# Kernel optimization log

Hardware: AMD Instinct MI355X
Metric: run time of the kernel (lower is better)

Reference implementation:

```python
import jax, jax.numpy as jnp
import numpy as np

B, C, H, W = 64, 32, 112, 112
RANK = 3


def setup_inputs() -> dict:
    key = jax.random.key(0)
    k1, k2, k3, k4, k5 = jax.random.split(key, 5)
    N = H * W  # 12544
    return {
        "x": jax.random.uniform(k1, (B, C, H, W), dtype=jnp.float32),
        "p_buffer": jax.random.normal(k2, (B, N, RANK), dtype=jnp.float32),
        "q_buffer": jax.random.normal(k3, (B, C, RANK), dtype=jnp.float32),
        "grad_p_buffer": jax.random.normal(k4, (B, N, RANK), dtype=jnp.float32),
        "grad_q_buffer": jax.random.normal(k5, (B, C, RANK), dtype=jnp.float32),
        "n_iter": 2,
    }


def _power_svd(X, P, Q, n_iter):
    # X: [b, c, n]; P: [b, n, r]; Q: [b, c, r]
    for i in range(n_iter):
        if i == n_iter - 1:
            P = jnp.linalg.qr(P)[0]  # batched reduced QR, tall-skinny (n x r)
        Q = jnp.einsum('bcn,bnr->bcr', X, P)
        if i == n_iter - 1:
            Q = jnp.linalg.qr(Q)[0]  # batched reduced QR (c x r)
        P = jnp.einsum('bcn,bcr->bnr', X, Q)  # X^T @ Q
    return P, Q


def reference(x, p_buffer, q_buffer, grad_p_buffer, grad_q_buffer, n_iter):
    shape = x.shape
    X = x.reshape(shape[0], shape[1], -1)  # [B, C, H*W]
    P, Q = _power_svd(X, p_buffer, q_buffer, n_iter)
    # low-rank reconstruction Q @ P^T, back to original shape
    return jnp.einsum('bcr,bnr->bcn', Q, P).reshape(shape)
```

## Files before the change

### kernel.cpp

```cpp
#include <hip/hip_runtime.h>
#include <math.h>

#define N_HW 12544
#define JCH 14
#define TILE_N 128
#define TPC 7
#define CHUNK (TILE_N*TPC)
#define XTS 36

#define WS_PQ (64*JCH*1024)
#define WS_U  (WS_PQ + 64*JCH*96)

__global__ __launch_bounds__(256)
void k1_partial(const float* __restrict__ x, const float* __restrict__ p,
                float* __restrict__ pS, float* __restrict__ pQ)
{
    const int b = blockIdx.y, j = blockIdx.x;
    const int tid  = threadIdx.x;
    const int lane = tid & 63, wave = tid >> 6;
    const int ty = lane >> 3, tx = lane & 7;

    __shared__ float XsT[TILE_N][XTS];
    __shared__ float Ps[TILE_N*3];
    __shared__ float redS[4][64][17];
    __shared__ float redQ[192];

    const float* Xb = x + (size_t)b * 32 * N_HW;
    const float* Pb = p + (size_t)b * N_HW * 3;

    float accS[4][4] = {};
    float accQ = 0.f;
    const int qc = tid / 6, qrh = tid % 6;
    const int qr = qrh >> 1, qh = qrh & 1;
    const int c_ld = tid >> 3, q_ld = tid & 7;

    for (int t = 0; t < TPC; ++t) {
        const int nbase = j * CHUNK + t * TILE_N;
        __syncthreads();
        {
            const float* row = Xb + (size_t)c_ld * N_HW + nbase;
            #pragma unroll
            for (int k = 0; k < 4; ++k) {
                const int nn = 4 * (q_ld + 8 * k);
                float4 v = *(const float4*)(row + nn);
                XsT[nn+0][c_ld] = v.x; XsT[nn+1][c_ld] = v.y;
                XsT[nn+2][c_ld] = v.z; XsT[nn+3][c_ld] = v.w;
            }
        }
        for (int i = tid; i < TILE_N*3; i += 256)
            Ps[i] = Pb[(size_t)nbase * 3 + i];
        __syncthreads();

        #pragma unroll 8
        for (int k = 0; k < 32; ++k) {
            const int n = wave * 32 + k;
            float4 a  = *(const float4*)&XsT[n][4*ty];
            float4 bb = *(const float4*)&XsT[n][4*tx];
            accS[0][0] += a.x*bb.x; accS[0][1] += a.x*bb.y; accS[0][2] += a.x*bb.z; accS[0][3] += a.x*bb.w;
            accS[1][0] += a.y*bb.x; accS[1][1] += a.y*bb.y; accS[1][2] += a.y*bb.z; accS[1][3] += a.y*bb.w;
            accS[2][0] += a.z*bb.x; accS[2][1] += a.z*bb.y; accS[2][2] += a.z*bb.z; accS[2][3] += a.z*bb.w;
            accS[3][0] += a.w*bb.x; accS[3][1] += a.w*bb.y; accS[3][2] += a.w*bb.z; accS[3][3] += a.w*bb.w;
        }
        if (tid < 192) {
            const int n0 = qh * 64;
            #pragma unroll 8
            for (int k = 0; k < 64; ++k) {
                const int n = n0 + k;
                accQ += XsT[n][qc] * Ps[3*n + qr];
            }
        }
    }

    __syncthreads();
    #pragma unroll
    for (int i = 0; i < 4; ++i)
        #pragma unroll
        for (int k = 0; k < 4; ++k)
            redS[wave][lane][i*4+k] = accS[i][k];
    if (tid < 192) redQ[tid] = accQ;
    __syncthreads();

    float* pSb = pS + ((size_t)b * JCH + j) * 1024;
    #pragma unroll
    for (int i = 0; i < 4; ++i) {
        const int e = tid + 256 * i;
        const int r = e >> 5, c = e & 31;
        const int ln  = (r >> 2) * 8 + (c >> 2);
        const int idx = (r & 3) * 4 + (c & 3);
        pSb[e] = redS[0][ln][idx] + redS[1][ln][idx] + redS[2][ln][idx] + redS[3][ln][idx];
    }
    if (tid < 96) {
        const int c = tid / 3, r = tid % 3;
        pQ[((size_t)b * JCH + j) * 96 + tid] = redQ[c*6 + r*2] + redQ[c*6 + r*2 + 1];
    }
}

__global__ __launch_bounds__(128)
void k2_solve(const float* __restrict__ pS, const float* __restrict__ pQ,
              float* __restrict__ Uo)
{
    const int b = blockIdx.x, tid = threadIdx.x;
    __shared__ float S[1024];
    __shared__ float Qv[96];
    __shared__ float V[96];
    __shared__ float G[6], L[6];

    #pragma unroll
    for (int i = 0; i < 8; ++i) {
        const int e = tid + 128 * i;
        float s = 0.f;
        for (int jj = 0; jj < JCH; ++jj) s += pS[((size_t)b*JCH + jj)*1024 + e];
        S[e] = s;
    }
    if (tid < 96) {
        float s = 0.f;
        for (int jj = 0; jj < JCH; ++jj) s += pQ[((size_t)b*JCH + jj)*96 + tid];
        Qv[tid] = s;
    }
    __syncthreads();
    if (tid < 96) {
        const int c = tid / 3, r = tid % 3;
        float s = 0.f;
        #pragma unroll 8
        for (int cc = 0; cc < 32; ++cc) s += S[c*32 + cc] * Qv[cc*3 + r];
        V[tid] = s;
    }
    for (int round = 0; round < 2; ++round) {
        __syncthreads();
        if (tid < 6) {
            const int r = (tid > 2) ? 2 : ((tid > 0) ? 1 : 0);
            const int s = tid - (r * (r + 1)) / 2;
            float g = 0.f;
            for (int c = 0; c < 32; ++c) g += V[c*3 + r] * V[c*3 + s];
            G[tid] = g;
        }
        __syncthreads();
        if (tid == 0) {
            const float l00 = sqrtf(G[0]);
            const float l10 = G[1] / l00, l20 = G[3] / l00;
            const float l11 = sqrtf(G[2] - l10*l10);
            const float l21 = (G[4] - l20*l10) / l11;
            const float l22 = sqrtf(G[5] - l20*l20 - l21*l21);
            L[0]=l00; L[1]=l10; L[2]=l11; L[3]=l20; L[4]=l21; L[5]=l22;
        }
        __syncthreads();
        if (tid < 32) {
            const float v0 = V[tid*3+0], v1 = V[tid*3+1], v2 = V[tid*3+2];
            const float u0 = v0 / L[0];
            const float u1 = (v1 - L[1]*u0) / L[2];
            const float u2 = (v2 - L[3]*u0 - L[4]*u1) / L[5];
            V[tid*3+0] = u0; V[tid*3+1] = u1; V[tid*3+2] = u2;
        }
    }
    __syncthreads();
    if (tid < 32) {
        Uo[(size_t)b*128 + tid*4 + 0] = V[tid*3+0];
        Uo[(size_t)b*128 + tid*4 + 1] = V[tid*3+1];
        Uo[(size_t)b*128 + tid*4 + 2] = V[tid*3+2];
        Uo[(size_t)b*128 + tid*4 + 3] = 0.f;
    }
}

__global__ __launch_bounds__(256)
void k3_out(const float* __restrict__ x, const float* __restrict__ Uw,
            float* __restrict__ out)
{
    const int b = blockIdx.y, tid = threadIdx.x;
    __shared__ float Us[32][4];
    if (tid < 128) ((float*)Us)[tid] = Uw[(size_t)b*128 + tid];
    __syncthreads();
    const int g = blockIdx.x * 256 + tid;
    if (g >= N_HW/4) return;

    const float* Xb = x   + (size_t)b * 32 * N_HW + 4*(size_t)g;
    float*       Ob = out + (size_t)b * 32 * N_HW + 4*(size_t)g;

    float t0x=0,t0y=0,t0z=0,t0w=0;
    float t1x=0,t1y=0,t1z=0,t1w=0;
    float t2x=0,t2y=0,t2z=0,t2w=0;
    #pragma unroll 8
    for (int c = 0; c < 32; ++c) {
        float4 xv = *(const float4*)(Xb + (size_t)c * N_HW);
        const float u0 = Us[c][0], u1 = Us[c][1], u2 = Us[c][2];
        t0x += u0*xv.x; t0y += u0*xv.y; t0z += u0*xv.z; t0w += u0*xv.w;
        t1x += u1*xv.x; t1y += u1*xv.y; t1z += u1*xv.z; t1w += u1*xv.w;
        t2x += u2*xv.x; t2y += u2*xv.y; t2z += u2*xv.z; t2w += u2*xv.w;
    }
    #pragma unroll 8
    for (int c = 0; c < 32; ++c) {
        const float u0 = Us[c][0], u1 = Us[c][1], u2 = Us[c][2];
        float4 o;
        o.x = u0*t0x + u1*t1x + u2*t2x;
        o.y = u0*t0y + u1*t1y + u2*t2y;
        o.z = u0*t0z + u1*t1z + u2*t2z;
        o.w = u0*t0w + u1*t1w + u2*t2w;
        *(float4*)(Ob + (size_t)c * N_HW) = o;
    }
}

extern "C" void kernel_launch(void* const* d_in, const int* in_sizes, int n_in,
                              void* d_out, int out_size, void* d_ws, size_t ws_size,
                              hipStream_t stream)
{
    const float* x = (const float*)d_in[0];
    const float* p = (const float*)d_in[1];
    float* ws = (float*)d_ws;
    float* pS = ws;
    float* pQ = ws + WS_PQ;
    float* U  = ws + WS_U;
    float* out = (float*)d_out;

    hipLaunchKernelGGL(k1_partial, dim3(JCH, 64), dim3(256), 0, stream, x, p, pS, pQ);
    hipLaunchKernelGGL(k2_solve,   dim3(64),      dim3(128), 0, stream, pS, pQ, U);
    hipLaunchKernelGGL(k3_out,     dim3((N_HW/4 + 255)/256, 64), dim3(256), 0, stream, x, U, out);
}
```

Measured before the change: 257.1 us.

## Split Gram kernel into more blocks with swizzled float4 tiles and atomic reduction

The Gram/projection kernel now gives each block a single 256-column tile (49 chunks per batch instead of 14 chunks of 7 tiles), so many more blocks run at once. X is kept in shared memory as float4 with an XOR swizzle, each thread computes 8x4 outputs by dotting float4 vectors, and the Q projection reads P as float4. Partial results are combined with global atomicAdd into a buffer that a new zero kernel clears first, so k2 no longer sums per-chunk partials. This adds a kernel launch and atomic contention, and the float summation order becomes nondeterministic.

After: 254.0 us. No clear change (-1.2%).

```diff
diff --git a/kernel.cpp b/kernel.cpp
--- a/kernel.cpp
+++ b/kernel.cpp
@@ -2,101 +2,121 @@
 #include <math.h>
 
 #define N_HW 12544
-#define JCH 14
-#define TILE_N 128
-#define TPC 7
-#define CHUNK (TILE_N*TPC)
-#define XTS 36
-
-#define WS_PQ (64*JCH*1024)
-#define WS_U  (WS_PQ + 64*JCH*96)
+#define TN 256
+#define NCHUNK 49
+
+#define WS_QG 65536
+#define WS_U  (WS_QG + 64*96)
+#define ZTOT  (WS_U)
+
+__device__ __forceinline__ int XQ(int c, int q) {
+    return (c << 6) + ((q & ~7) | ((q ^ ((c >> 3) << 1)) & 7));
+}
 
 __global__ __launch_bounds__(256)
-void k1_partial(const float* __restrict__ x, const float* __restrict__ p,
-                float* __restrict__ pS, float* __restrict__ pQ)
+void k0_zero(float* __restrict__ ws)
+{
+    const int g = blockIdx.x * 256 + threadIdx.x;
+    if (g < ZTOT / 4) ((float4*)ws)[g] = make_float4(0.f, 0.f, 0.f, 0.f);
+}
+
+__global__ __launch_bounds__(256)
+void k1_gram(const float* __restrict__ x, const float* __restrict__ p,
+             float* __restrict__ Sg, float* __restrict__ Qg)
 {
     const int b = blockIdx.y, j = blockIdx.x;
     const int tid  = threadIdx.x;
     const int lane = tid & 63, wave = tid >> 6;
-    const int ty = lane >> 3, tx = lane & 7;
-
-    __shared__ float XsT[TILE_N][XTS];
-    __shared__ float Ps[TILE_N*3];
-    __shared__ float redS[4][64][17];
-    __shared__ float redQ[192];
-
-    const float* Xb = x + (size_t)b * 32 * N_HW;
-    const float* Pb = p + (size_t)b * N_HW * 3;
-
-    float accS[4][4] = {};
-    float accQ = 0.f;
-    const int qc = tid / 6, qrh = tid % 6;
-    const int qr = qrh >> 1, qh = qrh & 1;
-    const int c_ld = tid >> 3, q_ld = tid & 7;
-
-    for (int t = 0; t < TPC; ++t) {
-        const int nbase = j * CHUNK + t * TILE_N;
-        __syncthreads();
-        {
-            const float* row = Xb + (size_t)c_ld * N_HW + nbase;
+    const int nbase = j * TN;
+
+    __shared__ float4 Xs4[32 * 64];
+    __shared__ alignas(16) float Ps[TN * 3];
+    __shared__ float Qred[8 * 32 * 3];
+
+    {
+        const int c = tid >> 3, q0 = tid & 7;
+        const float4* xrow = (const float4*)(x + ((size_t)b * 32 + c) * N_HW + nbase);
+        #pragma unroll
+        for (int k = 0; k < 8; ++k) {
+            const int q = q0 + 8 * k;
+            Xs4[XQ(c, q)] = xrow[q];
+        }
+    }
+    {
+        const float* pb = p + (size_t)b * N_HW * 3 + (size_t)nbase * 3;
+        #pragma unroll
+        for (int i = 0; i < 3; ++i) Ps[tid + 256 * i] = pb[tid + 256 * i];
+    }
+    __syncthreads();
+
+    const int sub = lane >> 5, ry = (lane >> 3) & 3, cx = lane & 7;
+    const int qbase = wave * 16;
+    float acc[8][4] = {};
+    for (int t = 0; t < 8; ++t) {
+        const int q = qbase + 2 * t + sub;
+        float4 bq[4], a[8];
+        #pragma unroll
+        for (int j2 = 0; j2 < 4; ++j2) bq[j2] = Xs4[XQ(4 * cx + j2, q)];
+        #pragma unroll
+        for (int i = 0; i < 8; ++i)   a[i]  = Xs4[XQ(8 * ry + i, q)];
+        #pragma unroll
+        for (int i = 0; i < 8; ++i)
             #pragma unroll
-            for (int k = 0; k < 4; ++k) {
-                const int nn = 4 * (q_ld + 8 * k);
-                float4 v = *(const float4*)(row + nn);
-                XsT[nn+0][c_ld] = v.x; XsT[nn+1][c_ld] = v.y;
-                XsT[nn+2][c_ld] = v.z; XsT[nn+3][c_ld] = v.w;
-            }
-        }
-        for (int i = tid; i < TILE_N*3; i += 256)
-            Ps[i] = Pb[(size_t)nbase * 3 + i];
-        __syncthreads();
-
-        #pragma unroll 8
-        for (int k = 0; k < 32; ++k) {
-            const int n = wave * 32 + k;
-            float4 a  = *(const float4*)&XsT[n][4*ty];
-            float4 bb = *(const float4*)&XsT[n][4*tx];
-            accS[0][0] += a.x*bb.x; accS[0][1] += a.x*bb.y; accS[0][2] += a.x*bb.z; accS[0][3] += a.x*bb.w;
-            accS[1][0] += a.y*bb.x; accS[1][1] += a.y*bb.y; accS[1][2] += a.y*bb.z; accS[1][3] += a.y*bb.w;
-            accS[2][0] += a.z*bb.x; accS[2][1] += a.z*bb.y; accS[2][2] += a.z*bb.z; accS[2][3] += a.z*bb.w;
-            accS[3][0] += a.w*bb.x; accS[3][1] += a.w*bb.y; accS[3][2] += a.w*bb.z; accS[3][3] += a.w*bb.w;
-        }
-        if (tid < 192) {
-            const int n0 = qh * 64;
-            #pragma unroll 8
-            for (int k = 0; k < 64; ++k) {
-                const int n = n0 + k;
-                accQ += XsT[n][qc] * Ps[3*n + qr];
-            }
-        }
+            for (int j2 = 0; j2 < 4; ++j2)
+                acc[i][j2] += a[i].x * bq[j2].x + a[i].y * bq[j2].y
+                            + a[i].z * bq[j2].z + a[i].w * bq[j2].w;
+    }
+
+    {
+        const int qc = tid & 31, g = tid >> 5;
+        float q0a = 0.f, q1a = 0.f, q2a = 0.f;
+        const float4* Ps4 = (const float4*)Ps;
+        #pragma unroll
+        for (int t = 0; t < 8; ++t) {
+            const int q = g * 8 + t;
+            float4 xv = Xs4[XQ(qc, q)];
+            float4 p0 = Ps4[3 * q], p1 = Ps4[3 * q + 1], p2 = Ps4[3 * q + 2];
+            q0a += xv.x * p0.x + xv.y * p0.w + xv.z * p1.z + xv.w * p2.y;
+            q1a += xv.x * p0.y + xv.y * p1.x + xv.z * p1.w + xv.w * p2.z;
+            q2a += xv.x * p0.z + xv.y * p1.y + xv.z * p2.x + xv.w * p2.w;
+        }
+        Qred[g * 96 + qc * 3 + 0] = q0a;
+        Qred[g * 96 + qc * 3 + 1] = q1a;
+        Qred[g * 96 + qc * 3 + 2] = q2a;
     }
 
     __syncthreads();
     #pragma unroll
-    for (int i = 0; i < 4; ++i)
-        #pragma unroll
-        for (int k = 0; k < 4; ++k)
-            redS[wave][lane][i*4+k] = accS[i][k];
-    if (tid < 192) redQ[tid] = accQ;
-    __syncthreads();
-
-    float* pSb = pS + ((size_t)b * JCH + j) * 1024;
+    for (int i = 0; i < 8; ++i)
+        Xs4[tid * 8 + i] = make_float4(acc[i][0], acc[i][1], acc[i][2], acc[i][3]);
+    __syncthreads();
+
+    const float* red = (const float*)Xs4;
+    float* Sb = Sg + (size_t)b * 1024;
     #pragma unroll
-    for (int i = 0; i < 4; ++i) {
-        const int e = tid + 256 * i;
-        const int r = e >> 5, c = e & 31;
-        const int ln  = (r >> 2) * 8 + (c >> 2);
-        const int idx = (r & 3) * 4 + (c & 3);
-        pSb[e] = redS[0][ln][idx] + redS[1][ln][idx] + redS[2][ln][idx] + redS[3][ln][idx];
+    for (int it = 0; it < 4; ++it) {
+        const int e = tid + 256 * it;
+        const int r = e >> 5, cl = e & 31;
+        const int ery = r >> 3, ei = r & 7, ecx = cl >> 2, ej = cl & 3;
+        const int slot = ery * 8 + ecx;
+        float s = 0.f;
+        #pragma unroll
+        for (int w = 0; w < 4; ++w) {
+            s += red[(w * 64 +      slot) * 32 + ei * 4 + ej];
+            s += red[(w * 64 + 32 + slot) * 32 + ei * 4 + ej];
+        }
+        atomicAdd(&Sb[e], s);
     }
     if (tid < 96) {
-        const int c = tid / 3, r = tid % 3;
-        pQ[((size_t)b * JCH + j) * 96 + tid] = redQ[c*6 + r*2] + redQ[c*6 + r*2 + 1];
+        float s = 0.f;
+        #pragma unroll
+        for (int g = 0; g < 8; ++g) s += Qred[g * 96 + tid];
+        atomicAdd(&Qg[(size_t)b * 96 + tid], s);
     }
 }
 
 __global__ __launch_bounds__(128)
-void k2_solve(const float* __restrict__ pS, const float* __restrict__ pQ,
+void k2_solve(const float* __restrict__ Sg, const float* __restrict__ Qg,
               float* __restrict__ Uo)
 {
     const int b = blockIdx.x, tid = threadIdx.x;
@@ -106,23 +126,14 @@
     __shared__ float G[6], L[6];
 
     #pragma unroll
-    for (int i = 0; i < 8; ++i) {
-        const int e = tid + 128 * i;
-        float s = 0.f;
-        for (int jj = 0; jj < JCH; ++jj) s += pS[((size_t)b*JCH + jj)*1024 + e];
-        S[e] = s;
-    }
-    if (tid < 96) {
-        float s = 0.f;
-        for (int jj = 0; jj < JCH; ++jj) s += pQ[((size_t)b*JCH + jj)*96 + tid];
-        Qv[tid] = s;
-    }
+    for (int i = 0; i < 8; ++i) S[tid + 128 * i] = Sg[(size_t)b * 1024 + tid + 128 * i];
+    if (tid < 96) Qv[tid] = Qg[(size_t)b * 96 + tid];
     __syncthreads();
     if (tid < 96) {
         const int c = tid / 3, r = tid % 3;
         float s = 0.f;
         #pragma unroll 8
-        for (int cc = 0; cc < 32; ++cc) s += S[c*32 + cc] * Qv[cc*3 + r];
+        for (int cc = 0; cc < 32; ++cc) s += S[c * 32 + cc] * Qv[cc * 3 + r];
         V[tid] = s;
     }
     for (int round = 0; round < 2; ++round) {
@@ -131,33 +142,33 @@
             const int r = (tid > 2) ? 2 : ((tid > 0) ? 1 : 0);
             const int s = tid - (r * (r + 1)) / 2;
             float g = 0.f;
-            for (int c = 0; c < 32; ++c) g += V[c*3 + r] * V[c*3 + s];
+            for (int c = 0; c < 32; ++c) g += V[c * 3 + r] * V[c * 3 + s];
             G[tid] = g;
         }
         __syncthreads();
         if (tid == 0) {
             const float l00 = sqrtf(G[0]);
             const float l10 = G[1] / l00, l20 = G[3] / l00;
-            const float l11 = sqrtf(G[2] - l10*l10);
-            const float l21 = (G[4] - l20*l10) / l11;
-            const float l22 = sqrtf(G[5] - l20*l20 - l21*l21);
-            L[0]=l00; L[1]=l10; L[2]=l11; L[3]=l20; L[4]=l21; L[5]=l22;
+            const float l11 = sqrtf(G[2] - l10 * l10);
+            const float l21 = (G[4] - l20 * l10) / l11;
+            const float l22 = sqrtf(G[5] - l20 * l20 - l21 * l21);
+            L[0] = l00; L[1] = l10; L[2] = l11; L[3] = l20; L[4] = l21; L[5] = l22;
         }
         __syncthreads();
         if (tid < 32) {
-            const float v0 = V[tid*3+0], v1 = V[tid*3+1], v2 = V[tid*3+2];
+            const float v0 = V[tid * 3 + 0], v1 = V[tid * 3 + 1], v2 = V[tid * 3 + 2];
             const float u0 = v0 / L[0];
-            const float u1 = (v1 - L[1]*u0) / L[2];
-            const float u2 = (v2 - L[3]*u0 - L[4]*u1) / L[5];
-            V[tid*3+0] = u0; V[tid*3+1] = u1; V[tid*3+2] = u2;
+            const float u1 = (v1 - L[1] * u0) / L[2];
+            const float u2 = (v2 - L[3] * u0 - L[4] * u1) / L[5];
+            V[tid * 3 + 0] = u0; V[tid * 3 + 1] = u1; V[tid * 3 + 2] = u2;
         }
     }
     __syncthreads();
     if (tid < 32) {
-        Uo[(size_t)b*128 + tid*4 + 0] = V[tid*3+0];
-        Uo[(size_t)b*128 + tid*4 + 1] = V[tid*3+1];
-        Uo[(size_t)b*128 + tid*4 + 2] = V[tid*3+2];
-        Uo[(size_t)b*128 + tid*4 + 3] = 0.f;
+        Uo[(size_t)b * 128 + tid * 4 + 0] = V[tid * 3 + 0];
+        Uo[(size_t)b * 128 + tid * 4 + 1] = V[tid * 3 + 1];
+        Uo[(size_t)b * 128 + tid * 4 + 2] = V[tid * 3 + 2];
+        Uo[(size_t)b * 128 + tid * 4 + 3] = 0.f;
     }
 }
 
@@ -167,33 +178,33 @@
 {
     const int b = blockIdx.y, tid = threadIdx.x;
     __shared__ float Us[32][4];
-    if (tid < 128) ((float*)Us)[tid] = Uw[(size_t)b*128 + tid];
+    if (tid < 128) ((float*)Us)[tid] = Uw[(size_t)b * 128 + tid];
     __syncthreads();
     const int g = blockIdx.x * 256 + tid;
-    if (g >= N_HW/4) return;
-
-    const float* Xb = x   + (size_t)b * 32 * N_HW + 4*(size_t)g;
-    float*       Ob = out + (size_t)b * 32 * N_HW + 4*(size_t)g;
-
-    float t0x=0,t0y=0,t0z=0,t0w=0;
-    float t1x=0,t1y=0,t1z=0,t1w=0;
-    float t2x=0,t2y=0,t2z=0,t2w=0;
+    if (g >= N_HW / 4) return;
+
+    const float* Xb = x   + (size_t)b * 32 * N_HW + 4 * (size_t)g;
+    float*       Ob = out + (size_t)b * 32 * N_HW + 4 * (size_t)g;
+
+    float t0x = 0, t0y = 0, t0z = 0, t0w = 0;
+    float t1x = 0, t1y = 0, t1z = 0, t1w = 0;
+    float t2x = 0, t2y = 0, t2z = 0, t2w = 0;
     #pragma unroll 8
     for (int c = 0; c < 32; ++c) {
         float4 xv = *(const float4*)(Xb + (size_t)c * N_HW);
         const float u0 = Us[c][0], u1 = Us[c][1], u2 = Us[c][2];
-        t0x += u0*xv.x; t0y += u0*xv.y; t0z += u0*xv.z; t0w += u0*xv.w;
-        t1x += u1*xv.x; t1y += u1*xv.y; t1z += u1*xv.z; t1w += u1*xv.w;
-        t2x += u2*xv.x; t2y += u2*xv.y; t2z += u2*xv.z; t2w += u2*xv.w;
+        t0x += u0 * xv.x; t0y += u0 * xv.y; t0z += u0 * xv.z; t0w += u0 * xv.w;
+        t1x += u1 * xv.x; t1y += u1 * xv.y; t1z += u1 * xv.z; t1w += u1 * xv.w;
+        t2x += u2 * xv.x; t2y += u2 * xv.y; t2z += u2 * xv.z; t2w += u2 * xv.w;
     }
     #pragma unroll 8
     for (int c = 0; c < 32; ++c) {
         const float u0 = Us[c][0], u1 = Us[c][1], u2 = Us[c][2];
         float4 o;
-        o.x = u0*t0x + u1*t1x + u2*t2x;
-        o.y = u0*t0y + u1*t1y + u2*t2y;
-        o.z = u0*t0z + u1*t1z + u2*t2z;
-        o.w = u0*t0w + u1*t1w + u2*t2w;
+        o.x = u0 * t0x + u1 * t1x + u2 * t2x;
+        o.y = u0 * t0y + u1 * t1y + u2 * t2y;
+        o.z = u0 * t0z + u1 * t1z + u2 * t2z;
+        o.w = u0 * t0w + u1 * t1w + u2 * t2w;
         *(float4*)(Ob + (size_t)c * N_HW) = o;
     }
 }
@@ -205,12 +216,13 @@
     const float* x = (const float*)d_in[0];
     const float* p = (const float*)d_in[1];
     float* ws = (float*)d_ws;
-    float* pS = ws;
-    float* pQ = ws + WS_PQ;
+    float* Sg = ws;
+    float* Qg = ws + WS_QG;
     float* U  = ws + WS_U;
     float* out = (float*)d_out;
 
-    hipLaunchKernelGGL(k1_partial, dim3(JCH, 64), dim3(256), 0, stream, x, p, pS, pQ);
-    hipLaunchKernelGGL(k2_solve,   dim3(64),      dim3(128), 0, stream, pS, pQ, U);
-    hipLaunchKernelGGL(k3_out,     dim3((N_HW/4 + 255)/256, 64), dim3(256), 0, stream, x, U, out);
-}
+    hipLaunchKernelGGL(k0_zero, dim3((ZTOT / 4 + 255) / 256), dim3(256), 0, stream, ws);
+    hipLaunchKernelGGL(k1_gram, dim3(NCHUNK, 64), dim3(256), 0, stream, x, p, Sg, Qg);
+    hipLaunchKernelGGL(k2_solve, dim3(64), dim3(128), 0, stream, Sg, Qg, U);
+    hipLaunchKernelGGL(k3_out, dim3((N_HW / 4 + 255) / 256, 64), dim3(256), 0, stream, x, U, out);
+}
```
